# Optimization experiments

Measured on AMD Instinct MI355X. Metric: run time of the kernel, lower is better.

Reference implementation:

```python
import jax, jax.numpy as jnp
import numpy as np

D = 1024          # d_model == d_memory
N_LAYERS = 4      # memory MLP depth
EPS = 1e-5        # LayerNorm epsilon (no scale/bias in original)


def _layernorm(x):
    mu = jnp.mean(x, axis=-1, keepdims=True)
    var = jnp.var(x, axis=-1, keepdims=True)
    return (x - mu) * jax.lax.rsqrt(var + EPS)


def setup_inputs() -> dict:
    key = jax.random.key(0)
    ks = jax.random.split(key, 8)
    x = jax.random.normal(ks[0], (4, 4096, D), dtype=jnp.float32)
    # projection params (normal std 0.02, zero bias, matching flax init)
    wq = jax.random.normal(ks[1], (D, D), dtype=jnp.float32) * 0.02
    bq = jnp.zeros((D,), dtype=jnp.float32)
    w_out = jax.random.normal(ks[2], (D, D), dtype=jnp.float32) * 0.02
    b_out = jnp.zeros((D,), dtype=jnp.float32)
    # memory MLP: 4 layers, all D x D (d_in = d_hidden = d_out = D), stacked
    mlp_w = jax.random.normal(ks[3], (N_LAYERS, D, D), dtype=jnp.float32) * 0.02
    mlp_b = jnp.zeros((N_LAYERS, D), dtype=jnp.float32)
    return {"x": x, "wq": wq, "bq": bq, "mlp_w": mlp_w, "mlp_b": mlp_b,
            "w_out": w_out, "b_out": b_out}


def reference(x, wq, bq, mlp_w, mlp_b, w_out, b_out):
    # retrieve(): y = W_out( M*(LN(W_Q(x))) + straight-through(q_norm) )
    q = jnp.einsum("bsd,de->bse", x, wq) + bq
    q_norm = _layernorm(q)
    # memory MLP weights get stop_gradient in the original
    mw = jax.lax.stop_gradient(mlp_w)
    mb = jax.lax.stop_gradient(mlp_b)
    h = q_norm
    for i in range(N_LAYERS):
        h = jnp.einsum("bsd,de->bse", h, mw[i]) + mb[i]
        if i < N_LAYERS - 1:
            h = jax.nn.silu(h)
    # straight-through trick: zero in the forward, passes grad to q_norm
    out = h + (q_norm - jax.lax.stop_gradient(q_norm))
    return jnp.einsum("bsd,de->bse", out, w_out) + b_out
```

## Files before the change

kernel.cpp:

```cpp
#include <hip/hip_runtime.h>
#include <hip/hip_bf16.h>
#include <math.h>

#define D_MODEL 1024
#define DD (1024 * 1024)

typedef unsigned short ushort_t;
using short8 = __attribute__((ext_vector_type(8))) short;
using f32x4  = __attribute__((ext_vector_type(4))) float;

#define ACT_NONE 0
#define ACT_SILU 1

__device__ __forceinline__ float bf2f(ushort_t u) {
    return __uint_as_float(((unsigned int)u) << 16);
}
__device__ __forceinline__ ushort_t f2bf(float f) {
    unsigned int x = __float_as_uint(f);
    x += 0x7fffu + ((x >> 16) & 1u);
    return (ushort_t)(x >> 16);
}

#define GL2LDS(gp, lp)                                                         \
    __builtin_amdgcn_global_load_lds(                                          \
        (const __attribute__((address_space(1))) void*)(gp),                   \
        (__attribute__((address_space(3))) void*)(lp), 16, 0, 0)

template <int ACT, int OUTF32, int BIASF>
__global__ __launch_bounds__(512, 2) void gemm256(
    const ushort_t* __restrict__ A,
    const ushort_t* __restrict__ Bt,
    const float* __restrict__ bias,
    void* __restrict__ Cv, int M)
{
    constexpr int K = 1024, N = 1024;
    constexpr int NU = K / 32;
    __shared__ ushort_t lds[4 * 16384];

    const int tid  = threadIdx.x;
    const int lane = tid & 63;
    const int wave = tid >> 6;
    const int quad = lane >> 4;
    const int lr   = lane & 15;
    const int wm   = wave >> 2;
    const int wn   = wave & 3;
    const int bm   = blockIdx.x;
    const int bn   = blockIdx.y;

    const ushort_t* Ab = A  + (size_t)bm * 256 * K;
    const ushort_t* Bb = Bt + (size_t)bn * 256 * K;

    const int sg    = (tid & 3) ^ ((tid >> 3) & 3);
    const size_t s0 = (size_t)(tid >> 2) * K + (size_t)sg * 8;
    const size_t s1 = s0 + (size_t)128 * K;
    const int d0 = tid * 8;
    const int d1 = tid * 8 + 4096;

    const int chk  = quad ^ ((lr >> 1) & 3);
    const int aoff = (wm * 128 + lr) * 32 + chk * 8;
    const int boff = (wn * 64  + lr) * 32 + chk * 8;

    short8 bfr[4], afrE[4], afrO[4];
    f32x4 acc[8][4];
#pragma unroll
    for (int i = 0; i < 8; i++)
#pragma unroll
        for (int j = 0; j < 4; j++) acc[i][j] = (f32x4){0.f, 0.f, 0.f, 0.f};

#define SA(v) do { const int b_ = ((v) & 3) * 16384;                           \
        GL2LDS(Ab + s0 + (v) * 32, lds + b_ + d0);                             \
        GL2LDS(Ab + s1 + (v) * 32, lds + b_ + d1); } while (0)
#define SB(v) do { const int b_ = ((v) & 3) * 16384 + 8192;                    \
        GL2LDS(Bb + s0 + (v) * 32, lds + b_ + d0);                             \
        GL2LDS(Bb + s1 + (v) * 32, lds + b_ + d1); } while (0)
#define RAE(v) do { const ushort_t* p_ = lds + ((v) & 3) * 16384 + aoff;       \
        afrE[0] = *(const short8*)(p_);                                        \
        afrE[1] = *(const short8*)(p_ + 512);                                  \
        afrE[2] = *(const short8*)(p_ + 1024);                                 \
        afrE[3] = *(const short8*)(p_ + 1536); } while (0)
#define RAO(v) do { const ushort_t* p_ = lds + ((v) & 3) * 16384 + aoff + 2048;\
        afrO[0] = *(const short8*)(p_);                                        \
        afrO[1] = *(const short8*)(p_ + 512);                                  \
        afrO[2] = *(const short8*)(p_ + 1024);                                 \
        afrO[3] = *(const short8*)(p_ + 1536); } while (0)
#define RB(v) do { const ushort_t* p_ = lds + ((v) & 3) * 16384 + 8192 + boff; \
        bfr[0] = *(const short8*)(p_);                                         \
        bfr[1] = *(const short8*)(p_ + 512);                                   \
        bfr[2] = *(const short8*)(p_ + 1024);                                  \
        bfr[3] = *(const short8*)(p_ + 1536); } while (0)

    SA(0); SB(0);
    SA(1); SB(1);
    SA(2); SB(2);
    asm volatile("s_waitcnt vmcnt(8)" ::: "memory");
    __builtin_amdgcn_s_barrier();
    RAE(0);
    RB(0);
    __builtin_amdgcn_sched_barrier(0);

#pragma unroll
    for (int u = 0; u < NU; ++u) {
        RAO(u);
        asm volatile("s_waitcnt vmcnt(4)" ::: "memory");
        __builtin_amdgcn_s_barrier();
        if (u + 3 < NU) SA(u + 3);
        asm volatile("s_waitcnt lgkmcnt(4)" ::: "memory");
        __builtin_amdgcn_sched_barrier(0);
        __builtin_amdgcn_s_setprio(1);
#pragma unroll
        for (int mt = 0; mt < 4; mt++)
#pragma unroll
            for (int nt = 0; nt < 4; nt++)
                acc[mt][nt] = __builtin_amdgcn_mfma_f32_16x16x32_bf16(
                    afrE[mt], bfr[nt], acc[mt][nt], 0, 0, 0);
        __builtin_amdgcn_s_setprio(0);
        if (u + 1 < NU) RAE(u + 1);
        asm volatile("s_waitcnt vmcnt(4)" ::: "memory");
        __builtin_amdgcn_s_barrier();
        if (u + 3 < NU) SB(u + 3);
        if (u + 1 < NU)
            asm volatile("s_waitcnt lgkmcnt(4)" ::: "memory");
        else
            asm volatile("s_waitcnt lgkmcnt(0)" ::: "memory");
        __builtin_amdgcn_sched_barrier(0);
        __builtin_amdgcn_s_setprio(1);
#pragma unroll
        for (int mt = 0; mt < 4; mt++)
#pragma unroll
            for (int nt = 0; nt < 4; nt++)
                acc[mt + 4][nt] = __builtin_amdgcn_mfma_f32_16x16x32_bf16(
                    afrO[mt], bfr[nt], acc[mt + 4][nt], 0, 0, 0);
        __builtin_amdgcn_s_setprio(0);
        if (u + 1 < NU) {
            RB(u + 1);
            __builtin_amdgcn_sched_barrier(0);
        }
    }
#undef SA
#undef SB
#undef RAE
#undef RAO
#undef RB

    float bv[4];
#pragma unroll
    for (int nt = 0; nt < 4; nt++)
        bv[nt] = BIASF ? bias[bn * 256 + wn * 64 + nt * 16 + lr] : 0.f;

#pragma unroll
    for (int mt = 0; mt < 8; mt++) {
#pragma unroll
        for (int nt = 0; nt < 4; nt++) {
            const int col = bn * 256 + wn * 64 + nt * 16 + lr;
#pragma unroll
            for (int r = 0; r < 4; r++) {
                const int row = bm * 256 + wm * 128 + mt * 16 + quad * 4 + r;
                float v = acc[mt][nt][r] + bv[nt];
                if (ACT == ACT_SILU) v = v / (1.f + __expf(-v));
                if (OUTF32)
                    ((float*)Cv)[(size_t)row * N + col] = v;
                else
                    ((ushort_t*)Cv)[(size_t)row * N + col] = f2bf(v);
            }
        }
    }
}

template <int ACT, int OUTF32, int BIASF>
__global__ __launch_bounds__(256) void gemm_bf16(
    const ushort_t* __restrict__ A,
    const ushort_t* __restrict__ Bt,
    const float* __restrict__ bias,
    void* __restrict__ Cv, int M)
{
    constexpr int K = 1024, N = 1024;
    __shared__ ushort_t As[128 * 32];
    __shared__ ushort_t Bs[128 * 32];

    const int tid  = threadIdx.x;
    const int lane = tid & 63;
    const int wave = tid >> 6;
    const int quad = lane >> 4;
    const int lr   = lane & 15;
    const int bm   = blockIdx.x;
    const int bn   = blockIdx.y;
    const int wm   = (wave >> 1) * 64;
    const int wn   = (wave & 1) * 64;

    f32x4 acc[4][4];
#pragma unroll
    for (int i = 0; i < 4; i++)
#pragma unroll
        for (int j = 0; j < 4; j++) acc[i][j] = (f32x4){0.f, 0.f, 0.f, 0.f};

    int ci0 = tid, ci1 = tid + 256;
    int am0 = ci0 >> 2, akc0 = (ci0 & 3) ^ ((am0 >> 1) & 3);
    int am1 = ci1 >> 2, akc1 = (ci1 & 3) ^ ((am1 >> 1) & 3);
    const ushort_t* Ab = A + (size_t)(bm * 128) * K;
    const ushort_t* Bb = Bt + (size_t)(bn * 128) * K;

    for (int k0 = 0; k0 < K; k0 += 32) {
        GL2LDS(Ab + (size_t)am0 * K + k0 + akc0 * 8, As + ci0 * 8);
        GL2LDS(Ab + (size_t)am1 * K + k0 + akc1 * 8, As + ci1 * 8);
        GL2LDS(Bb + (size_t)am0 * K + k0 + akc0 * 8, Bs + ci0 * 8);
        GL2LDS(Bb + (size_t)am1 * K + k0 + akc1 * 8, Bs + ci1 * 8);
        __syncthreads();

        short8 af[4], bfr[4];
#pragma unroll
        for (int t = 0; t < 4; t++) {
            int m = wm + t * 16 + lr;
            af[t] = *(const short8*)(As + m * 32 + ((quad ^ ((m >> 1) & 3)) * 8));
            int n = wn + t * 16 + lr;
            bfr[t] = *(const short8*)(Bs + n * 32 + ((quad ^ ((n >> 1) & 3)) * 8));
        }
#pragma unroll
        for (int mt = 0; mt < 4; mt++)
#pragma unroll
            for (int nt = 0; nt < 4; nt++)
                acc[mt][nt] = __builtin_amdgcn_mfma_f32_16x16x32_bf16(
                    af[mt], bfr[nt], acc[mt][nt], 0, 0, 0);
        __syncthreads();
    }

    float bv[4];
#pragma unroll
    for (int nt = 0; nt < 4; nt++)
        bv[nt] = BIASF ? bias[bn * 128 + wn + nt * 16 + lr] : 0.f;

#pragma unroll
    for (int mt = 0; mt < 4; mt++) {
#pragma unroll
        for (int nt = 0; nt < 4; nt++) {
            const int col = bn * 128 + wn + nt * 16 + lr;
#pragma unroll
            for (int r = 0; r < 4; r++) {
                const int row = bm * 128 + wm + mt * 16 + quad * 4 + r;
                float v = acc[mt][nt][r] + bv[nt];
                if (ACT == ACT_SILU) v = v / (1.f + __expf(-v));
                if (OUTF32)
                    ((float*)Cv)[(size_t)row * N + col] = v;
                else
                    ((ushort_t*)Cv)[(size_t)row * N + col] = f2bf(v);
            }
        }
    }
}

__global__ __launch_bounds__(256) void layernorm_bf16(ushort_t* __restrict__ X)
{
    const int row = blockIdx.x;
    const int tid = threadIdx.x;
    ushort_t* x = X + (size_t)row * D_MODEL + tid * 4;

    uint2 u = *(uint2*)x;
    float a = bf2f(u.x & 0xffff), b = bf2f(u.x >> 16);
    float c = bf2f(u.y & 0xffff), d = bf2f(u.y >> 16);
    float s = a + b + c + d;
    float ss = a * a + b * b + c * c + d * d;

#pragma unroll
    for (int off = 32; off > 0; off >>= 1) {
        s += __shfl_down(s, off);
        ss += __shfl_down(ss, off);
    }
    __shared__ float sbuf[4], ssbuf[4];
    const int wave = tid >> 6;
    if ((tid & 63) == 0) { sbuf[wave] = s; ssbuf[wave] = ss; }
    __syncthreads();
    const float S = sbuf[0] + sbuf[1] + sbuf[2] + sbuf[3];
    const float SS = ssbuf[0] + ssbuf[1] + ssbuf[2] + ssbuf[3];
    const float mu = S * (1.f / D_MODEL);
    const float var = SS * (1.f / D_MODEL) - mu * mu;
    const float r = rsqrtf(var + 1e-5f);

    a = (a - mu) * r; b = (b - mu) * r; c = (c - mu) * r; d = (d - mu) * r;
    u.x = (unsigned)f2bf(a) | ((unsigned)f2bf(b) << 16);
    u.y = (unsigned)f2bf(c) | ((unsigned)f2bf(d) << 16);
    *(uint2*)x = u;
}

__global__ __launch_bounds__(256) void prep_all(
    const float* __restrict__ wq, const float* __restrict__ mlp_w,
    const float* __restrict__ w_out, const float* __restrict__ x,
    const float* __restrict__ b3, const float* __restrict__ bout,
    ushort_t* __restrict__ wt, ushort_t* __restrict__ Q,
    float* __restrict__ bf, int nxblk)
{
    const int blk = blockIdx.x;
    const int tid = threadIdx.x;

    if (blk < 6144) {
        const int z = blk >> 10;
        const int t = blk & 1023;
        const int k0 = (t >> 5) * 32;
        const int n0 = (t & 31) * 32;
        const int r = tid >> 5;
        const int c = tid & 31;

        if (z == 5) {
            const float* src = mlp_w + (size_t)3 * DD;
            ushort_t* dst = wt + (size_t)5 * DD;
#pragma unroll
            for (int i = 0; i < 4; i++) {
                size_t idx = (size_t)(k0 + r + 8 * i) * D_MODEL + n0 + c;
                dst[idx] = f2bf(src[idx]);
            }
            return;
        }
        const float* src = (z == 0) ? wq : (z < 4) ? (mlp_w + (size_t)(z - 1) * DD) : w_out;
        ushort_t* dst = wt + (size_t)z * DD;
        __shared__ float tile[32][33];
#pragma unroll
        for (int i = 0; i < 4; i++)
            tile[r + 8 * i][c] = src[(size_t)(k0 + r + 8 * i) * D_MODEL + n0 + c];
        __syncthreads();
#pragma unroll
        for (int i = 0; i < 4; i++)
            dst[(size_t)(n0 + r + 8 * i) * D_MODEL + k0 + c] = f2bf(tile[c][r + 8 * i]);
        return;
    }
    if (blk < 6144 + nxblk) {
        int i = (blk - 6144) * 256 + tid;
        const float4* p = (const float4*)(x + (size_t)i * 8);
        float4 v0 = p[0], v1 = p[1];
        union { ushort_t u[8]; uint4 v; } pk;
        pk.u[0] = f2bf(v0.x); pk.u[1] = f2bf(v0.y);
        pk.u[2] = f2bf(v0.z); pk.u[3] = f2bf(v0.w);
        pk.u[4] = f2bf(v1.x); pk.u[5] = f2bf(v1.y);
        pk.u[6] = f2bf(v1.z); pk.u[7] = f2bf(v1.w);
        *(uint4*)(Q + (size_t)i * 8) = pk.v;
        return;
    }
    {
        const int b = blk - 6144 - nxblk;
        const int n = b * 32 + (tid & 31);
        const int kg = tid >> 5;
        float s = 0.f;
        for (int k = kg * 128; k < (kg + 1) * 128; k++)
            s = fmaf(b3[k], w_out[(size_t)k * D_MODEL + n], s);
        __shared__ float red[8][32];
        red[kg][tid & 31] = s;
        __syncthreads();
        if (kg == 0) {
            float t = 0.f;
#pragma unroll
            for (int j = 0; j < 8; j++) t += red[j][tid & 31];
            bf[n] = t + bout[n];
        }
    }
}

extern "C" void kernel_launch(void* const* d_in, const int* in_sizes, int n_in,
                              void* d_out, int out_size, void* d_ws, size_t ws_size,
                              hipStream_t stream)
{
    const float* x     = (const float*)d_in[0];
    const float* wq    = (const float*)d_in[1];
    const float* bq    = (const float*)d_in[2];
    const float* mlp_w = (const float*)d_in[3];
    const float* mlp_b = (const float*)d_in[4];
    const float* w_out = (const float*)d_in[5];
    const float* b_out = (const float*)d_in[6];

    const int D = D_MODEL;
    const int M = in_sizes[0] / D;

    ushort_t* wt  = (ushort_t*)d_ws;
    ushort_t* w3b = wt + (size_t)5 * DD;
    ushort_t* wtF = wt + (size_t)6 * DD;
    ushort_t* Q   = wt + (size_t)7 * DD;
    float*    bf  = (float*)(Q + (size_t)M * D);
    ushort_t* P   = (ushort_t*)d_out;

    const int nxblk = M * D / 2048;
    prep_all<<<6144 + nxblk + 32, 256, 0, stream>>>(
        wq, mlp_w, w_out, x, mlp_b + 3 * D, b_out, wt, Q, bf, nxblk);
    gemm_bf16<ACT_NONE, 0, 0><<<dim3(8, 8), 256, 0, stream>>>(
        wt + (size_t)4 * DD, w3b, nullptr, wtF, 1024);

    if ((M & 255) == 0) {
        dim3 grid(M / 256, D / 256);
        gemm256<ACT_NONE, 0, 1><<<grid, 512, 0, stream>>>(Q, wt + (size_t)0 * DD, bq, P, M);
        layernorm_bf16<<<M, 256, 0, stream>>>(P);
        gemm256<ACT_SILU, 0, 1><<<grid, 512, 0, stream>>>(P, wt + (size_t)1 * DD, mlp_b + 0 * D, Q, M);
        gemm256<ACT_SILU, 0, 1><<<grid, 512, 0, stream>>>(Q, wt + (size_t)2 * DD, mlp_b + 1 * D, P, M);
        gemm256<ACT_SILU, 0, 1><<<grid, 512, 0, stream>>>(P, wt + (size_t)3 * DD, mlp_b + 2 * D, Q, M);
        gemm256<ACT_NONE, 1, 1><<<grid, 512, 0, stream>>>(Q, wtF, bf, d_out, M);
    } else {
        dim3 grid(M / 128, D / 128);
        gemm_bf16<ACT_NONE, 0, 1><<<grid, 256, 0, stream>>>(Q, wt + (size_t)0 * DD, bq, P, M);
        layernorm_bf16<<<M, 256, 0, stream>>>(P);
        gemm_bf16<ACT_SILU, 0, 1><<<grid, 256, 0, stream>>>(P, wt + (size_t)1 * DD, mlp_b + 0 * D, Q, M);
        gemm_bf16<ACT_SILU, 0, 1><<<grid, 256, 0, stream>>>(Q, wt + (size_t)2 * DD, mlp_b + 1 * D, P, M);
        gemm_bf16<ACT_SILU, 0, 1><<<grid, 256, 0, stream>>>(P, wt + (size_t)3 * DD, mlp_b + 2 * D, Q, M);
        gemm_bf16<ACT_NONE, 1, 1><<<grid, 256, 0, stream>>>(Q, wtF, bf, d_out, M);
    }
}
```

Before: 354.5 us.

## Fold LayerNorm into GEMM epilogues via row stats and column-sum correction

Removes the standalone LayerNorm kernel. The first GEMM now accumulates per-row sum and sum-of-squares with shuffles and atomics. The next GEMM applies the normalization algebraically in its epilogue as rin*acc - rin*mu*colsum(W) + b, with the weight column sums precomputed in the prep kernel. This saves one full read and write pass over the activation tensor, at the cost of atomics and a less numerically exact normalization, since the GEMM consumes the un-normalized bf16 activations.

New measurement: 434.8 us, median of 2. 22.7% more time.

```diff
diff --git a/kernel.cpp b/kernel.cpp
--- a/kernel.cpp
+++ b/kernel.cpp
@@ -26,12 +26,13 @@
         (const __attribute__((address_space(1))) void*)(gp),                   \
         (__attribute__((address_space(3))) void*)(lp), 16, 0, 0)
 
-template <int ACT, int OUTF32, int BIASF>
+template <int ACT, int OUTF32, int BIASF, int STATS, int LNAFF>
 __global__ __launch_bounds__(512, 2) void gemm256(
     const ushort_t* __restrict__ A,
     const ushort_t* __restrict__ Bt,
     const float* __restrict__ bias,
-    void* __restrict__ Cv, int M)
+    void* __restrict__ Cv, int M,
+    float* __restrict__ stats, const float* __restrict__ csw)
 {
     constexpr int K = 1024, N = 1024;
     constexpr int NU = K / 32;
@@ -142,25 +143,51 @@
 #undef RAO
 #undef RB
 
-    float bv[4];
-#pragma unroll
-    for (int nt = 0; nt < 4; nt++)
-        bv[nt] = BIASF ? bias[bn * 256 + wn * 64 + nt * 16 + lr] : 0.f;
+    float bv[4], cw[4];
+#pragma unroll
+    for (int nt = 0; nt < 4; nt++) {
+        const int col = bn * 256 + wn * 64 + nt * 16 + lr;
+        bv[nt] = BIASF ? bias[col] : 0.f;
+        cw[nt] = LNAFF ? csw[col] : 0.f;
+    }
 
 #pragma unroll
     for (int mt = 0; mt < 8; mt++) {
 #pragma unroll
-        for (int nt = 0; nt < 4; nt++) {
-            const int col = bn * 256 + wn * 64 + nt * 16 + lr;
-#pragma unroll
-            for (int r = 0; r < 4; r++) {
-                const int row = bm * 256 + wm * 128 + mt * 16 + quad * 4 + r;
-                float v = acc[mt][nt][r] + bv[nt];
+        for (int r = 0; r < 4; r++) {
+            const int row = bm * 256 + wm * 128 + mt * 16 + quad * 4 + r;
+            float rin = 1.f, rmu = 0.f;
+            if (LNAFF) {
+                const float2 st = *(const float2*)(stats + 2 * (size_t)row);
+                const float mu  = st.x * (1.f / D_MODEL);
+                const float var = st.y * (1.f / D_MODEL) - mu * mu;
+                rin = rsqrtf(var + 1e-5f);
+                rmu = rin * mu;
+            }
+            float s4 = 0.f, ss4 = 0.f;
+#pragma unroll
+            for (int nt = 0; nt < 4; nt++) {
+                const int col = bn * 256 + wn * 64 + nt * 16 + lr;
+                float v = acc[mt][nt][r];
+                if (LNAFF) v = rin * v - rmu * cw[nt] + bv[nt];
+                else       v = v + bv[nt];
+                if (STATS) { s4 += v; ss4 += v * v; }
                 if (ACT == ACT_SILU) v = v / (1.f + __expf(-v));
                 if (OUTF32)
                     ((float*)Cv)[(size_t)row * N + col] = v;
                 else
                     ((ushort_t*)Cv)[(size_t)row * N + col] = f2bf(v);
+            }
+            if (STATS) {
+#pragma unroll
+                for (int m_ = 1; m_ < 16; m_ <<= 1) {
+                    s4  += __shfl_xor(s4,  m_);
+                    ss4 += __shfl_xor(ss4, m_);
+                }
+                if (lr == 0) {
+                    atomicAdd(stats + 2 * (size_t)row,     s4);
+                    atomicAdd(stats + 2 * (size_t)row + 1, ss4);
+                }
             }
         }
     }
@@ -285,7 +312,8 @@
     const float* __restrict__ w_out, const float* __restrict__ x,
     const float* __restrict__ b3, const float* __restrict__ bout,
     ushort_t* __restrict__ wt, ushort_t* __restrict__ Q,
-    float* __restrict__ bf, int nxblk)
+    float* __restrict__ bf, float* __restrict__ stats,
+    float* __restrict__ csw, int nxblk)
 {
     const int blk = blockIdx.x;
     const int tid = threadIdx.x;
@@ -332,9 +360,9 @@
         *(uint4*)(Q + (size_t)i * 8) = pk.v;
         return;
     }
-    {
-        const int b = blk - 6144 - nxblk;
-        const int n = b * 32 + (tid & 31);
+    const int t = blk - 6144 - nxblk;
+    if (t < 32) {
+        const int n = t * 32 + (tid & 31);
         const int kg = tid >> 5;
         float s = 0.f;
         for (int k = kg * 128; k < (kg + 1) * 128; k++)
@@ -343,11 +371,35 @@
         red[kg][tid & 31] = s;
         __syncthreads();
         if (kg == 0) {
-            float t = 0.f;
-#pragma unroll
-            for (int j = 0; j < 8; j++) t += red[j][tid & 31];
-            bf[n] = t + bout[n];
-        }
+            float tt = 0.f;
+#pragma unroll
+            for (int j = 0; j < 8; j++) tt += red[j][tid & 31];
+            bf[n] = tt + bout[n];
+        }
+        return;
+    }
+    if (t < 64) {
+        const int b = t - 32;
+        const int n = b * 32 + (tid & 31);
+        const int kg = tid >> 5;
+        float s = 0.f;
+        for (int k = kg * 128; k < (kg + 1) * 128; k++)
+            s += mlp_w[(size_t)k * D_MODEL + n];
+        __shared__ float red2[8][32];
+        red2[kg][tid & 31] = s;
+        __syncthreads();
+        if (kg == 0) {
+            float tt = 0.f;
+#pragma unroll
+            for (int j = 0; j < 8; j++) tt += red2[j][tid & 31];
+            csw[n] = tt;
+        }
+        return;
+    }
+    {
+        const int b = t - 64;
+        *(float4*)(stats + (size_t)b * 1024 + tid * 4) =
+            (float4){0.f, 0.f, 0.f, 0.f};
     }
 }
 
@@ -366,27 +418,34 @@
     const int D = D_MODEL;
     const int M = in_sizes[0] / D;
 
-    ushort_t* wt  = (ushort_t*)d_ws;
-    ushort_t* w3b = wt + (size_t)5 * DD;
-    ushort_t* wtF = wt + (size_t)6 * DD;
-    ushort_t* Q   = wt + (size_t)7 * DD;
-    float*    bf  = (float*)(Q + (size_t)M * D);
-    ushort_t* P   = (ushort_t*)d_out;
+    ushort_t* wt    = (ushort_t*)d_ws;
+    ushort_t* w3b   = wt + (size_t)5 * DD;
+    ushort_t* wtF   = wt + (size_t)6 * DD;
+    ushort_t* Q     = wt + (size_t)7 * DD;
+    float*    bf    = (float*)(Q + (size_t)M * D);
+    ushort_t* P     = (ushort_t*)d_out;
+    float*    ob    = (float*)d_out;
+    float*    stats = ob + (size_t)M * D / 2;
+    float*    csw   = stats + 2 * (size_t)M;
 
     const int nxblk = M * D / 2048;
-    prep_all<<<6144 + nxblk + 32, 256, 0, stream>>>(
-        wq, mlp_w, w_out, x, mlp_b + 3 * D, b_out, wt, Q, bf, nxblk);
+    prep_all<<<6144 + nxblk + 96, 256, 0, stream>>>(
+        wq, mlp_w, w_out, x, mlp_b + 3 * D, b_out, wt, Q, bf, stats, csw, nxblk);
     gemm_bf16<ACT_NONE, 0, 0><<<dim3(8, 8), 256, 0, stream>>>(
         wt + (size_t)4 * DD, w3b, nullptr, wtF, 1024);
 
     if ((M & 255) == 0) {
         dim3 grid(M / 256, D / 256);
-        gemm256<ACT_NONE, 0, 1><<<grid, 512, 0, stream>>>(Q, wt + (size_t)0 * DD, bq, P, M);
-        layernorm_bf16<<<M, 256, 0, stream>>>(P);
-        gemm256<ACT_SILU, 0, 1><<<grid, 512, 0, stream>>>(P, wt + (size_t)1 * DD, mlp_b + 0 * D, Q, M);
-        gemm256<ACT_SILU, 0, 1><<<grid, 512, 0, stream>>>(Q, wt + (size_t)2 * DD, mlp_b + 1 * D, P, M);
-        gemm256<ACT_SILU, 0, 1><<<grid, 512, 0, stream>>>(P, wt + (size_t)3 * DD, mlp_b + 2 * D, Q, M);
-        gemm256<ACT_NONE, 1, 1><<<grid, 512, 0, stream>>>(Q, wtF, bf, d_out, M);
+        gemm256<ACT_NONE, 0, 1, 1, 0><<<grid, 512, 0, stream>>>(
+            Q, wt + (size_t)0 * DD, bq, P, M, stats, nullptr);
+        gemm256<ACT_SILU, 0, 1, 0, 1><<<grid, 512, 0, stream>>>(
+            P, wt + (size_t)1 * DD, mlp_b + 0 * D, Q, M, stats, csw);
+        gemm256<ACT_SILU, 0, 1, 0, 0><<<grid, 512, 0, stream>>>(
+            Q, wt + (size_t)2 * DD, mlp_b + 1 * D, P, M, nullptr, nullptr);
+        gemm256<ACT_SILU, 0, 1, 0, 0><<<grid, 512, 0, stream>>>(
+            P, wt + (size_t)3 * DD, mlp_b + 2 * D, Q, M, nullptr, nullptr);
+        gemm256<ACT_NONE, 1, 1, 0, 0><<<grid, 512, 0, stream>>>(
+            Q, wtF, bf, d_out, M, nullptr, nullptr);
     } else {
         dim3 grid(M / 128, D / 128);
         gemm_bf16<ACT_NONE, 0, 1><<<grid, 256, 0, stream>>>(Q, wt + (size_t)0 * DD, bq, P, M);
```
